# Performance work log

Measured on AMD Instinct MI355X. Metric: run time of the kernel, lower is better.

Reference implementation:

```python
import jax, jax.numpy as jnp
import numpy as np

B, S, D, H, HD, MLP = 2, 4096, 512, 8, 64, 2048
BLK, C = 128, 32  # Fixed1Pattern(block_size=128), Fixed2Pattern(block_size=128, c=32)
EPS = 1e-6


def _xavier(key, shape, fan_in, fan_out):
    lim = np.sqrt(6.0 / (fan_in + fan_out)).astype(np.float32)
    return jax.random.uniform(key, shape, jnp.float32, -lim, lim)


def setup_inputs() -> dict:
    key = jax.random.key(0)
    ks = jax.random.split(key, 9)
    return {
        "inputs": jax.random.normal(ks[0], (B, S, D), jnp.float32),
        "ln1_scale": jnp.ones((D,), jnp.float32),
        "ln1_bias": jnp.zeros((D,), jnp.float32),
        "wq": _xavier(ks[1], (D, H, HD), D, H * HD),
        "wk": _xavier(ks[2], (D, H, HD), D, H * HD),
        "wv": _xavier(ks[3], (D, H, HD), D, H * HD),
        "wo": _xavier(ks[4], (H, HD, D), H * HD, D),
        "ln2_scale": jnp.ones((D,), jnp.float32),
        "ln2_bias": jnp.zeros((D,), jnp.float32),
        "w1": _xavier(ks[5], (D, MLP), D, MLP),
        "b1": jax.random.normal(ks[6], (MLP,), jnp.float32) * 1e-6,
        "w2": _xavier(ks[7], (MLP, D), MLP, D),
        "b2": jax.random.normal(ks[8], (D,), jnp.float32) * 1e-6,
    }


def _layer_norm(x, scale, bias):
    mu = jnp.mean(x, axis=-1, keepdims=True)
    var = jnp.mean(jnp.square(x - mu), axis=-1, keepdims=True)
    return (x - mu) * jax.lax.rsqrt(var + EPS) * scale + bias


def _sparse_mask():
    # Union of causal Fixed1 (same block) and Fixed2 (last C columns of each block) patterns.
    i = jnp.arange(S)[:, None]
    j = jnp.arange(S)[None, :]
    causal = j <= i
    local = (i // BLK) == (j // BLK)            # Fixed1: within-block
    strided = (j % BLK) >= (BLK - C)            # Fixed2: block-summary columns
    return causal & (local | strided)           # [S, S] bool


def reference(inputs, ln1_scale, ln1_bias, wq, wk, wv, wo,
              ln2_scale, ln2_bias, w1, b1, w2, b2):
    x = _layer_norm(inputs, ln1_scale, ln1_bias)
    q = jnp.einsum("bsd,dhk->bshk", x, wq)
    k = jnp.einsum("bsd,dhk->bshk", x, wk)
    v = jnp.einsum("bsd,dhk->bshk", x, wv)
    scale = 1.0 / np.sqrt(HD).astype(np.float32)
    scores = jnp.einsum("bqhk,bshk->bhqs", q * scale, k)  # [B,H,S,S]
    mask = _sparse_mask()[None, None]
    scores = jnp.where(mask, scores, jnp.float32(-1e9))
    attn = jax.nn.softmax(scores, axis=-1)
    ctx = jnp.einsum("bhqs,bshk->bqhk", attn, v)
    attn_out = jnp.einsum("bqhk,hkd->bqd", ctx, wo)
    x = attn_out + inputs  # residual 1 (dropout deterministic)
    y = _layer_norm(x, ln2_scale, ln2_bias)
    y = jax.nn.gelu(y @ w1 + b1) @ w2 + b2  # MlpBlock
    return x + y
```

## Files before the change

kernel.cpp:

```cpp
#include <hip/hip_runtime.h>
#include <hip/hip_bf16.h>

typedef __attribute__((ext_vector_type(8))) __bf16 bf16x8;
typedef __attribute__((ext_vector_type(8))) short s16x8;
typedef __attribute__((ext_vector_type(4))) float f32x4;

#define NB 2
#define NS 4096
#define ND 512
#define NH 8
#define NHD 64
#define NMLP 2048

__device__ __forceinline__ unsigned short f2b(float f) {
  __hip_bfloat16 h = __float2bfloat16(f);
  return __builtin_bit_cast(unsigned short, h);
}

__device__ __forceinline__ float geluf(float x) {
  float u = 0.7978845608028654f * (x + 0.044715f * x * x * x);
  return x / (1.0f + __expf(-2.0f * u));
}

__device__ __forceinline__ void gload16(const void* g, void* l) {
  __builtin_amdgcn_global_load_lds((const __attribute__((address_space(1))) void*)g,
                                   (__attribute__((address_space(3))) void*)l, 16, 0, 0);
}

__global__ __launch_bounds__(256) void prep_weights(const float* __restrict__ wq,
                                                    const float* __restrict__ wk,
                                                    const float* __restrict__ wv,
                                                    const float* __restrict__ wo,
                                                    const float* __restrict__ w1,
                                                    const float* __restrict__ w2,
                                                    unsigned short* __restrict__ qkvT,
                                                    unsigned short* __restrict__ woT,
                                                    unsigned short* __restrict__ w1T,
                                                    unsigned short* __restrict__ w2T) {
  __shared__ unsigned short lt[64][66];
  const int tile = blockIdx.x, t = threadIdx.x;
  const float* src;
  unsigned short* dst;
  int R, C, tr, tc;
  float sc = 1.0f;
  if (tile < 256) {
    int seg = tile >> 6, tt = tile & 63;
    R = 512; C = 512;
    src = seg == 0 ? wq : seg == 1 ? wk : seg == 2 ? wv : wo;
    dst = (seg < 3) ? (qkvT + ((size_t)seg << 18)) : woT;
    if (seg == 0) sc = 0.125f;
    tr = tt >> 3; tc = tt & 7;
  } else if (tile < 512) {
    int tt = tile - 256;
    R = 512; C = 2048; src = w1; dst = w1T;
    tr = tt >> 5; tc = tt & 31;
  } else {
    int tt = tile - 512;
    R = 2048; C = 512; src = w2; dst = w2T;
    tr = tt >> 3; tc = tt & 7;
  }
  const int r0 = tr * 64, c0 = tc * 64;
  const int fx = t & 15, fy = t >> 4;
#pragma unroll
  for (int p = 0; p < 4; ++p) {
    int rr = p * 16 + fy;
    float4 v = *(const float4*)&src[(size_t)(r0 + rr) * C + c0 + fx * 4];
    lt[rr][fx * 4 + 0] = f2b(v.x * sc);
    lt[rr][fx * 4 + 1] = f2b(v.y * sc);
    lt[rr][fx * 4 + 2] = f2b(v.z * sc);
    lt[rr][fx * 4 + 3] = f2b(v.w * sc);
  }
  __syncthreads();
#pragma unroll
  for (int p = 0; p < 4; ++p) {
    int cc = p * 16 + fy;
    ushort4 o;
    o.x = lt[fx * 4 + 0][cc];
    o.y = lt[fx * 4 + 1][cc];
    o.z = lt[fx * 4 + 2][cc];
    o.w = lt[fx * 4 + 3][cc];
    *(ushort4*)&dst[(size_t)(c0 + cc) * R + r0 + fx * 4] = o;
  }
}

__global__ __launch_bounds__(256) void ln_bf16(const float* __restrict__ x,
                                               const float* __restrict__ g,
                                               const float* __restrict__ bta,
                                               unsigned short* __restrict__ out) {
  const int t = threadIdx.x, l = t & 63, w = t >> 6;
  const size_t row = (size_t)blockIdx.x * 4 + w;
  const float4* xr = (const float4*)(x + row * ND);
  float4 a = xr[l];
  float4 bq = xr[64 + l];
  float s = a.x + a.y + a.z + a.w + bq.x + bq.y + bq.z + bq.w;
  float ss = a.x * a.x + a.y * a.y + a.z * a.z + a.w * a.w +
             bq.x * bq.x + bq.y * bq.y + bq.z * bq.z + bq.w * bq.w;
#pragma unroll
  for (int msk = 1; msk <= 32; msk <<= 1) {
    s += __shfl_xor(s, msk);
    ss += __shfl_xor(ss, msk);
  }
  float mu = s * (1.0f / ND);
  float var = ss * (1.0f / ND) - mu * mu;
  float rr = rsqrtf(var + 1e-6f);
  const float4* g4 = (const float4*)g;
  const float4* b4 = (const float4*)bta;
  float4 g0 = g4[l], g1 = g4[64 + l], b0 = b4[l], b1 = b4[64 + l];
  ushort4 o0, o1;
  o0.x = f2b((a.x - mu) * rr * g0.x + b0.x);
  o0.y = f2b((a.y - mu) * rr * g0.y + b0.y);
  o0.z = f2b((a.z - mu) * rr * g0.z + b0.z);
  o0.w = f2b((a.w - mu) * rr * g0.w + b0.w);
  o1.x = f2b((bq.x - mu) * rr * g1.x + b1.x);
  o1.y = f2b((bq.y - mu) * rr * g1.y + b1.y);
  o1.z = f2b((bq.z - mu) * rr * g1.z + b1.z);
  o1.w = f2b((bq.w - mu) * rr * g1.w + b1.w);
  ushort4* orow = (ushort4*)(out + row * ND);
  orow[l] = o0;
  orow[64 + l] = o1;
}

template <int EPI>
__global__ __launch_bounds__(512) void gemm_bt(const unsigned short* __restrict__ A,
                                               const unsigned short* __restrict__ Bt,
                                               int M, int N, int K,
                                               unsigned short* __restrict__ ob,
                                               float* __restrict__ of,
                                               const float* __restrict__ addf,
                                               const float* __restrict__ bias) {
  __shared__ unsigned short lA[2][128 * 64];
  __shared__ unsigned short lB[2][128 * 64];
  const int t = threadIdx.x;
  const int l = t & 63, w = t >> 6;
  const int wr = w >> 2, wc = w & 3;
  const int gx = gridDim.x;
  const int nwg = gx * gridDim.y;
  const int fid = blockIdx.y * gx + blockIdx.x;
  const int q8 = nwg >> 3, r8 = nwg & 7, xcd = fid & 7, idx = fid >> 3;
  const int lid = (xcd < r8 ? xcd * (q8 + 1) : r8 * (q8 + 1) + (xcd - r8) * q8) + idx;
  const int bm = lid / gx, bn = lid % gx;
  const size_t rowBytes = (size_t)K * 2;
  const char* Ab = (const char*)A + (size_t)bm * 128 * rowBytes;
  const char* Bb = (const char*)Bt + (size_t)bn * 128 * rowBytes;
  const int sr0 = t >> 3;
  const int scb = (((t & 7) ^ ((t >> 3) & 7)) << 4);
  f32x4 acc[4][2] = {};

  auto stage = [&](int buf, int k0) {
    char* dA = (char*)&lA[buf][0] + t * 16;
    char* dB = (char*)&lB[buf][0] + t * 16;
#pragma unroll
    for (int i = 0; i < 2; ++i) {
      const size_t go = (size_t)(sr0 + i * 64) * rowBytes + 2 * k0 + scb;
      gload16(Ab + go, dA + i * 8192);
      gload16(Bb + go, dB + i * 8192);
    }
  };

  const int nkt = K >> 6;
  stage(0, 0);
  int cur = 0;
  for (int kt = 0; kt < nkt; ++kt) {
    if (kt + 1 < nkt) {
      stage(cur ^ 1, (kt + 1) * 64);
      asm volatile("s_waitcnt vmcnt(4)" ::: "memory");
    } else {
      asm volatile("s_waitcnt vmcnt(0)" ::: "memory");
    }
    __builtin_amdgcn_s_barrier();
    __builtin_amdgcn_sched_barrier(0);
#pragma unroll
    for (int ks = 0; ks < 2; ++ks) {
      const int xg = ((ks * 4 + (l >> 4)) ^ (l & 7)) * 8;
      bf16x8 aF[4], bF[2];
#pragma unroll
      for (int m = 0; m < 4; ++m)
        aF[m] = *(const bf16x8*)&lA[cur][(wr * 64 + m * 16 + (l & 15)) * 64 + xg];
#pragma unroll
      for (int n = 0; n < 2; ++n)
        bF[n] = *(const bf16x8*)&lB[cur][(wc * 32 + n * 16 + (l & 15)) * 64 + xg];
      __builtin_amdgcn_s_setprio(1);
#pragma unroll
      for (int m = 0; m < 4; ++m)
#pragma unroll
        for (int n = 0; n < 2; ++n)
          acc[m][n] = __builtin_amdgcn_mfma_f32_16x16x32_bf16(aF[m], bF[n], acc[m][n], 0, 0, 0);
      __builtin_amdgcn_s_setprio(0);
    }
    asm volatile("s_waitcnt lgkmcnt(0)" ::: "memory");
    __builtin_amdgcn_s_barrier();
    cur ^= 1;
  }
#pragma unroll
  for (int m = 0; m < 4; ++m)
#pragma unroll
    for (int n = 0; n < 2; ++n) {
      int row0 = bm * 128 + wr * 64 + m * 16 + (l >> 4) * 4;
      int col = bn * 128 + wc * 32 + n * 16 + (l & 15);
      if constexpr (EPI == 0) {
        int part = col >> 9, nn = col & 511;
        int hh = nn >> 6, hd = nn & 63;
        int b = row0 >> 12, sidx0 = row0 & 4095;
        if (part < 2) {
#pragma unroll
          for (int j = 0; j < 4; ++j)
            ob[((((size_t)part * NB + b) * NH + hh) * NS + sidx0 + j) * NHD + hd] =
                f2b(acc[m][n][j]);
        } else {
          ushort4 o;
          o.x = f2b(acc[m][n][0]);
          o.y = f2b(acc[m][n][1]);
          o.z = f2b(acc[m][n][2]);
          o.w = f2b(acc[m][n][3]);
          *(ushort4*)&ob[(size_t)2 * NB * NH * NS * NHD +
                         (((size_t)b * NH + hh) * NHD + hd) * NS + sidx0] = o;
        }
      } else if constexpr (EPI == 2) {
#pragma unroll
        for (int j = 0; j < 4; ++j) {
          size_t i = (size_t)(row0 + j) * NMLP + col;
          ob[i] = f2b(geluf(acc[m][n][j] + bias[col]));
        }
      } else {
#pragma unroll
        for (int j = 0; j < 4; ++j) {
          int row = row0 + j;
          float v = acc[m][n][j];
          if constexpr (EPI == 1) {
            size_t i = (size_t)row * ND + col;
            of[i] = v + addf[i];
          } else {
            size_t i = (size_t)row * ND + col;
            of[i] = v + bias[col] + addf[i];
          }
        }
      }
    }
}

__global__ __launch_bounds__(512, 4) void attn_sparse(const unsigned short* __restrict__ qm,
                                                      const unsigned short* __restrict__ km,
                                                      const unsigned short* __restrict__ vTg,
                                                      unsigned short* __restrict__ ctx) {
  __shared__ unsigned short kl[128 * 72];
  __shared__ unsigned short vt[64 * 136];
  __shared__ unsigned short pl[8][16 * 72];
  const int t = threadIdx.x, l = t & 63, w = t >> 6;
  const int bid = blockIdx.x;
  const int hh = bid & 7;
  const int jj = bid >> 3;
  const int b = jj >> 5;
  const int qb = (jj < 32) ? jj : 63 - jj;
  const size_t bh = ((size_t)b * NH + hh) * NS;
  const size_t bhd = ((size_t)b * NH + hh) * NHD;
  const int qrow0 = qb * 128 + w * 16;
  bf16x8 qa[2];
#pragma unroll
  for (int ks = 0; ks < 2; ++ks)
    qa[ks] = *(const bf16x8*)&qm[(bh + qrow0 + (l & 15)) * NHD + ks * 32 + (l >> 4) * 8];
  f32x4 c[4] = {};
  float mrun[4], lrun[4];
#pragma unroll
  for (int j = 0; j < 4; ++j) { mrun[j] = -1e30f; lrun[j] = 0.0f; }

  const int nsum128 = qb >> 2, rem = qb & 3;
  const int nSumCh = nsum128 + (rem ? 1 : 0);
  const int nch = nSumCh + 1;
  const int kkey = t >> 2, kd = (t & 3) * 16;
  const int vd = t >> 3, vk = (t & 7) * 16;

  s16x8 kr0, kr1, vr0, vr1;
  auto issueLoads = [&](int c2) {
    int grK, sV;
    if (c2 < nSumCh) {
      grK = ((c2 << 2) + (kkey >> 5)) * 128 + 96 + (kkey & 31);
      sV = ((c2 << 2) + (vk >> 5)) * 128 + 96 + (vk & 31);
    } else {
      grK = qb * 128 + kkey;
      sV = qb * 128 + vk;
    }
    const unsigned short* kp = &km[(bh + grK) * NHD + kd];
    kr0 = *(const s16x8*)kp;
    kr1 = *(const s16x8*)(kp + 8);
    const unsigned short* vp = &vTg[(bhd + vd) * NS + sV];
    vr0 = *(const s16x8*)vp;
    vr1 = *(const s16x8*)(vp + 8);
  };

  issueLoads(0);
  for (int ch = 0; ch < nch; ++ch) {
    if (ch) {
      asm volatile("s_waitcnt lgkmcnt(0)" ::: "memory");
      __builtin_amdgcn_s_barrier();
    }
    *(s16x8*)&kl[kkey * 72 + kd] = kr0;
    *(s16x8*)&kl[kkey * 72 + kd + 8] = kr1;
    *(s16x8*)&vt[vd * 136 + vk] = vr0;
    *(s16x8*)&vt[vd * 136 + vk + 8] = vr1;
    asm volatile("s_waitcnt lgkmcnt(0)" ::: "memory");
    __builtin_amdgcn_s_barrier();
    __builtin_amdgcn_sched_barrier(0);
    if (ch + 1 < nch) issueLoads(ch + 1);

    const bool isLocal = (ch == nch - 1);
    const bool isRem = (rem != 0) && !isLocal && (ch == nsum128);
    const int nT = isLocal ? (w + 1) : (isRem ? 2 * rem : 8);
    const int nTpl = isLocal ? ((w | 1) + 1) : nT;
    const int nKs = nTpl >> 1;

    f32x4 sf[8];
#pragma unroll
    for (int n = 0; n < 8; ++n) {
      if (n < nT) {
        const bf16x8 k0 = *(const bf16x8*)&kl[(n * 16 + (l & 15)) * 72 + (l >> 4) * 8];
        const bf16x8 k1 = *(const bf16x8*)&kl[(n * 16 + (l & 15)) * 72 + 32 + (l >> 4) * 8];
        f32x4 a = {};
        a = __builtin_amdgcn_mfma_f32_16x16x32_bf16(qa[0], k0, a, 0, 0, 0);
        a = __builtin_amdgcn_mfma_f32_16x16x32_bf16(qa[1], k1, a, 0, 0, 0);
        if (isLocal && n == w) {
#pragma unroll
          for (int j = 0; j < 4; ++j)
            if ((l & 15) > (l >> 4) * 4 + j) a[j] = -1e9f;
        }
        sf[n] = a;
      }
    }
    float cm[4];
#pragma unroll
    for (int j = 0; j < 4; ++j) cm[j] = -1e30f;
#pragma unroll
    for (int n = 0; n < 8; ++n)
      if (n < nT)
#pragma unroll
        for (int j = 0; j < 4; ++j) cm[j] = fmaxf(cm[j], sf[n][j]);
#pragma unroll
    for (int j = 0; j < 4; ++j) {
      cm[j] = fmaxf(cm[j], __shfl_xor(cm[j], 1));
      cm[j] = fmaxf(cm[j], __shfl_xor(cm[j], 2));
      cm[j] = fmaxf(cm[j], __shfl_xor(cm[j], 4));
      cm[j] = fmaxf(cm[j], __shfl_xor(cm[j], 8));
    }
    bool need = false;
#pragma unroll
    for (int j = 0; j < 4; ++j) need |= (cm[j] > mrun[j] + 8.0f);
    if (__any(need)) {
      float al[4];
#pragma unroll
      for (int j = 0; j < 4; ++j) {
        float nm = fmaxf(mrun[j], cm[j]);
        al[j] = __expf(mrun[j] - nm);
        mrun[j] = nm;
      }
#pragma unroll
      for (int n = 0; n < 4; ++n)
#pragma unroll
        for (int j = 0; j < 4; ++j) c[n][j] *= al[j];
#pragma unroll
      for (int j = 0; j < 4; ++j) lrun[j] *= al[j];
    }
    float rs[4] = {0.f, 0.f, 0.f, 0.f};
#pragma unroll
    for (int n = 0; n < 8; ++n)
      if (n < nT)
#pragma unroll
        for (int j = 0; j < 4; ++j) {
          float p = __expf(sf[n][j] - mrun[j]);
          sf[n][j] = p;
          rs[j] += p;
        }
#pragma unroll
    for (int j = 0; j < 4; ++j) {
      rs[j] += __shfl_xor(rs[j], 1);
      rs[j] += __shfl_xor(rs[j], 2);
      rs[j] += __shfl_xor(rs[j], 4);
      rs[j] += __shfl_xor(rs[j], 8);
      lrun[j] += rs[j];
    }
#pragma unroll
    for (int h = 0; h < 2; ++h) {
      if (h * 4 < nTpl) {
#pragma unroll
        for (int n2 = 0; n2 < 4; ++n2) {
          const int n = h * 4 + n2;
#pragma unroll
          for (int j = 0; j < 4; ++j) {
            if (n < nTpl) {
              unsigned short pv = 0;
              if (n < nT) pv = f2b(sf[n][j]);
              pl[w][((l >> 4) * 4 + j) * 72 + n2 * 16 + (l & 15)] = pv;
            }
          }
        }
#pragma unroll
        for (int ks2 = 0; ks2 < 2; ++ks2) {
          const int ks = h * 2 + ks2;
          if (ks < nKs) {
            const bf16x8 pa = *(const bf16x8*)&pl[w][(l & 15) * 72 + ks2 * 32 + (l >> 4) * 8];
#pragma unroll
            for (int nd = 0; nd < 4; ++nd) {
              const bf16x8 vb =
                  *(const bf16x8*)&vt[(nd * 16 + (l & 15)) * 136 + ks * 32 + (l >> 4) * 8];
              c[nd] = __builtin_amdgcn_mfma_f32_16x16x32_bf16(pa, vb, c[nd], 0, 0, 0);
            }
          }
        }
      }
    }
  }
  float rinv[4];
#pragma unroll
  for (int j = 0; j < 4; ++j) rinv[j] = 1.0f / lrun[j];
#pragma unroll
  for (int n = 0; n < 4; ++n)
#pragma unroll
    for (int j = 0; j < 4; ++j) {
      int srow = qrow0 + (l >> 4) * 4 + j;
      int col = n * 16 + (l & 15);
      ctx[((size_t)b * NS + srow) * ND + hh * NHD + col] = f2b(c[n][j] * rinv[j]);
    }
}

extern "C" void kernel_launch(void* const* d_in, const int* in_sizes, int n_in,
                              void* d_out, int out_size, void* d_ws, size_t ws_size,
                              hipStream_t stream) {
  (void)in_sizes; (void)n_in; (void)out_size; (void)ws_size;
  const float* inputs = (const float*)d_in[0];
  const float* ln1s = (const float*)d_in[1];
  const float* ln1b = (const float*)d_in[2];
  const float* wq = (const float*)d_in[3];
  const float* wk = (const float*)d_in[4];
  const float* wv = (const float*)d_in[5];
  const float* wo = (const float*)d_in[6];
  const float* ln2s = (const float*)d_in[7];
  const float* ln2b = (const float*)d_in[8];
  const float* w1 = (const float*)d_in[9];
  const float* b1 = (const float*)d_in[10];
  const float* w2 = (const float*)d_in[11];
  const float* b2 = (const float*)d_in[12];
  float* out = (float*)d_out;

  unsigned short* xln = (unsigned short*)d_ws;
  unsigned short* xln2 = xln + (size_t)8192 * 512;
  unsigned short* ctx = xln2 + (size_t)8192 * 512;
  unsigned short* qkv = ctx + (size_t)8192 * 512;
  float* xres = (float*)(qkv + (size_t)3 * 8192 * 512);
  unsigned short* hbuf = (unsigned short*)(xres + (size_t)8192 * 512);
  unsigned short* qkvT = hbuf + (size_t)8192 * 2048;
  unsigned short* woT = qkvT + (size_t)1536 * 512;
  unsigned short* w1T = woT + (size_t)512 * 512;
  unsigned short* w2T = w1T + (size_t)2048 * 512;

  prep_weights<<<768, 256, 0, stream>>>(wq, wk, wv, wo, w1, w2, qkvT, woT, w1T, w2T);
  ln_bf16<<<2048, 256, 0, stream>>>(inputs, ln1s, ln1b, xln);
  gemm_bt<0><<<dim3(12, 64), 512, 0, stream>>>(xln, qkvT, 8192, 1536, 512,
                                               qkv, nullptr, nullptr, nullptr);
  attn_sparse<<<512, 512, 0, stream>>>(qkv, qkv + (size_t)8192 * 512,
                                       qkv + (size_t)2 * 8192 * 512, ctx);
  gemm_bt<1><<<dim3(4, 64), 512, 0, stream>>>(ctx, woT, 8192, 512, 512,
                                              nullptr, xres, inputs, nullptr);
  ln_bf16<<<2048, 256, 0, stream>>>(xres, ln2s, ln2b, xln2);
  gemm_bt<2><<<dim3(16, 64), 512, 0, stream>>>(xln2, w1T, 8192, 2048, 512,
                                               hbuf, nullptr, nullptr, b1);
  gemm_bt<3><<<dim3(4, 64), 512, 0, stream>>>(hbuf, w2T, 8192, 512, 2048,
                                              nullptr, out, xres, b2);
}
```

Before: 158.4 us.

## Double-buffer sparse attention K/V tiles with direct global-to-LDS loads and XOR swizzle

```diff
diff --git a/kernel.cpp b/kernel.cpp
--- a/kernel.cpp
+++ b/kernel.cpp
@@ -242,9 +242,9 @@
                                                       const unsigned short* __restrict__ km,
                                                       const unsigned short* __restrict__ vTg,
                                                       unsigned short* __restrict__ ctx) {
-  __shared__ unsigned short kl[128 * 72];
-  __shared__ unsigned short vt[64 * 136];
-  __shared__ unsigned short pl[8][16 * 72];
+  __shared__ unsigned short kl[2][128 * 64];
+  __shared__ unsigned short vt[2][64 * 128];
+  __shared__ unsigned short pl[8][16 * 64];
   const int t = threadIdx.x, l = t & 63, w = t >> 6;
   const int bid = blockIdx.x;
   const int hh = bid & 7;
@@ -266,41 +266,41 @@
   const int nsum128 = qb >> 2, rem = qb & 3;
   const int nSumCh = nsum128 + (rem ? 1 : 0);
   const int nch = nSumCh + 1;
-  const int kkey = t >> 2, kd = (t & 3) * 16;
-  const int vd = t >> 3, vk = (t & 7) * 16;
-
-  s16x8 kr0, kr1, vr0, vr1;
-  auto issueLoads = [&](int c2) {
-    int grK, sV;
-    if (c2 < nSumCh) {
-      grK = ((c2 << 2) + (kkey >> 5)) * 128 + 96 + (kkey & 31);
-      sV = ((c2 << 2) + (vk >> 5)) * 128 + 96 + (vk & 31);
+
+  const int kr_ = t >> 3;
+  const int ku_ = (t & 7) ^ (kr_ & 7);
+  const int vr_ = t >> 4;
+  const int vu_ = ((t & 15) & 8) | (((t & 15) & 7) ^ (vr_ & 7));
+
+  auto keyOf = [&](int c2, int kk) -> int {
+    return (c2 < nSumCh) ? ((c2 * 4 + (kk >> 5)) * 128 + 96 + (kk & 31)) : (qb * 128 + kk);
+  };
+  auto stage = [&](int buf, int c2) {
+    const int krow0 = keyOf(c2, kr_);
+    gload16(&km[(bh + krow0) * NHD + ku_ * 8], (char*)&kl[buf][0] + t * 16);
+    const int krow1 = keyOf(c2, kr_ + 64);
+    gload16(&km[(bh + krow1) * NHD + ku_ * 8], (char*)&kl[buf][0] + 8192 + t * 16);
+    const int gk = keyOf(c2, vu_ * 8);
+    gload16(&vTg[(bhd + vr_) * NS + gk], (char*)&vt[buf][0] + t * 16);
+    gload16(&vTg[(bhd + vr_ + 32) * NS + gk], (char*)&vt[buf][0] + 8192 + t * 16);
+  };
+
+  const int e_ = l & 7, q_ = l >> 4;
+  const int kx0 = (q_ ^ e_) * 8;
+  const int kx1 = ((4 + q_) ^ e_) * 8;
+  const int r4_ = (q_ & 1) << 2;
+
+  stage(0, 0);
+  int cur = 0;
+  for (int ch = 0; ch < nch; ++ch) {
+    if (ch + 1 < nch) {
+      stage(cur ^ 1, ch + 1);
+      asm volatile("s_waitcnt vmcnt(4)" ::: "memory");
     } else {
-      grK = qb * 128 + kkey;
-      sV = qb * 128 + vk;
-    }
-    const unsigned short* kp = &km[(bh + grK) * NHD + kd];
-    kr0 = *(const s16x8*)kp;
-    kr1 = *(const s16x8*)(kp + 8);
-    const unsigned short* vp = &vTg[(bhd + vd) * NS + sV];
-    vr0 = *(const s16x8*)vp;
-    vr1 = *(const s16x8*)(vp + 8);
-  };
-
-  issueLoads(0);
-  for (int ch = 0; ch < nch; ++ch) {
-    if (ch) {
-      asm volatile("s_waitcnt lgkmcnt(0)" ::: "memory");
-      __builtin_amdgcn_s_barrier();
-    }
-    *(s16x8*)&kl[kkey * 72 + kd] = kr0;
-    *(s16x8*)&kl[kkey * 72 + kd + 8] = kr1;
-    *(s16x8*)&vt[vd * 136 + vk] = vr0;
-    *(s16x8*)&vt[vd * 136 + vk + 8] = vr1;
-    asm volatile("s_waitcnt lgkmcnt(0)" ::: "memory");
+      asm volatile("s_waitcnt vmcnt(0)" ::: "memory");
+    }
     __builtin_amdgcn_s_barrier();
     __builtin_amdgcn_sched_barrier(0);
-    if (ch + 1 < nch) issueLoads(ch + 1);
 
     const bool isLocal = (ch == nch - 1);
     const bool isRem = (rem != 0) && !isLocal && (ch == nsum128);
@@ -312,15 +312,16 @@
 #pragma unroll
     for (int n = 0; n < 8; ++n) {
       if (n < nT) {
-        const bf16x8 k0 = *(const bf16x8*)&kl[(n * 16 + (l & 15)) * 72 + (l >> 4) * 8];
-        const bf16x8 k1 = *(const bf16x8*)&kl[(n * 16 + (l & 15)) * 72 + 32 + (l >> 4) * 8];
+        const int row = n * 16 + (l & 15);
+        const bf16x8 k0 = *(const bf16x8*)&kl[cur][row * 64 + kx0];
+        const bf16x8 k1 = *(const bf16x8*)&kl[cur][row * 64 + kx1];
         f32x4 a = {};
         a = __builtin_amdgcn_mfma_f32_16x16x32_bf16(qa[0], k0, a, 0, 0, 0);
         a = __builtin_amdgcn_mfma_f32_16x16x32_bf16(qa[1], k1, a, 0, 0, 0);
         if (isLocal && n == w) {
 #pragma unroll
           for (int j = 0; j < 4; ++j)
-            if ((l & 15) > (l >> 4) * 4 + j) a[j] = -1e9f;
+            if ((l & 15) > q_ * 4 + j) a[j] = -1e9f;
         }
         sf[n] = a;
       }
@@ -382,12 +383,14 @@
 #pragma unroll
         for (int n2 = 0; n2 < 4; ++n2) {
           const int n = h * 4 + n2;
+          const int cu = n2 * 2 + ((l >> 3) & 1);
 #pragma unroll
           for (int j = 0; j < 4; ++j) {
             if (n < nTpl) {
               unsigned short pv = 0;
               if (n < nT) pv = f2b(sf[n][j]);
-              pl[w][((l >> 4) * 4 + j) * 72 + n2 * 16 + (l & 15)] = pv;
+              const int rowp = q_ * 4 + j;
+              pl[w][rowp * 64 + (cu ^ (r4_ | j)) * 8 + e_] = pv;
             }
           }
         }
@@ -395,17 +398,21 @@
         for (int ks2 = 0; ks2 < 2; ++ks2) {
           const int ks = h * 2 + ks2;
           if (ks < nKs) {
-            const bf16x8 pa = *(const bf16x8*)&pl[w][(l & 15) * 72 + ks2 * 32 + (l >> 4) * 8];
+            const bf16x8 pa =
+                *(const bf16x8*)&pl[w][(l & 15) * 64 + (ks2 ? kx1 : kx0)];
 #pragma unroll
             for (int nd = 0; nd < 4; ++nd) {
-              const bf16x8 vb =
-                  *(const bf16x8*)&vt[(nd * 16 + (l & 15)) * 136 + ks * 32 + (l >> 4) * 8];
+              const bf16x8 vb = *(const bf16x8*)&vt[cur][(nd * 16 + (l & 15)) * 128 +
+                                                         ((ks & 2) << 5) +
+                                                         (ks2 ? kx1 : kx0)];
               c[nd] = __builtin_amdgcn_mfma_f32_16x16x32_bf16(pa, vb, c[nd], 0, 0, 0);
             }
           }
         }
       }
     }
+    __builtin_amdgcn_s_barrier();
+    cur ^= 1;
   }
   float rinv[4];
 #pragma unroll
@@ -414,7 +421,7 @@
   for (int n = 0; n < 4; ++n)
 #pragma unroll
     for (int j = 0; j < 4; ++j) {
-      int srow = qrow0 + (l >> 4) * 4 + j;
+      int srow = qrow0 + q_ * 4 + j;
       int col = n * 16 + (l & 15);
       ctx[((size_t)b * NS + srow) * ND + hh * NHD + col] = f2b(c[n][j] * rinv[j]);
     }
```

New measurement: 157.3 us. Within noise of the previous version (-0.7%).
